# Performance work log

Hardware: AMD Instinct MI355X
Metric: run time of the kernel (lower is better)

Reference implementation:

```python
import jax, jax.numpy as jnp
import numpy as np

B, T, A, H = 2048, 512, 32, 16


def setup_inputs() -> dict:
    key = jax.random.key(0)
    ks = jax.random.split(key, 10)
    s = 1.0 / np.sqrt(H)
    inputs = jax.random.normal(ks[0], (B, T, A), dtype=jnp.float32)
    masks = (jax.random.uniform(ks[1], (B, T)) > 0.05).astype(jnp.float32)
    h0 = jnp.zeros((1, B, H), dtype=jnp.float32)
    c0 = jnp.zeros((1, B, H), dtype=jnp.float32)
    # torch nn.LSTM params (gate order i,f,g,o) and linear heads
    w_ih = jax.random.uniform(ks[2], (4 * H, A), minval=-s, maxval=s)
    w_hh = jax.random.uniform(ks[3], (4 * H, H), minval=-s, maxval=s)
    b_ih = jax.random.uniform(ks[4], (4 * H,), minval=-s, maxval=s)
    b_hh = jax.random.uniform(ks[5], (4 * H,), minval=-s, maxval=s)
    w_actor = jax.random.uniform(ks[6], (A, H), minval=-s, maxval=s)
    b_actor = jax.random.uniform(ks[7], (A,), minval=-s, maxval=s)
    w_critic = jax.random.uniform(ks[8], (1, H), minval=-s, maxval=s)
    b_critic = jax.random.uniform(ks[9], (1,), minval=-s, maxval=s)
    return {"inputs": inputs, "masks": masks, "h0": h0, "c0": c0,
            "w_ih": w_ih, "w_hh": w_hh, "b_ih": b_ih, "b_hh": b_hh,
            "w_actor": w_actor, "b_actor": b_actor,
            "w_critic": w_critic, "b_critic": b_critic}


def reference(inputs, masks, h0, c0, w_ih, w_hh, b_ih, b_hh,
              w_actor, b_actor, w_critic, b_critic):
    # masked LSTM scan: state is zeroed where mask==0 before each step
    def step(carry, xm):
        h, c = carry                      # [B,H]
        x, m = xm                         # x:[B,A], m:[B]
        h = h * m[:, None]
        c = c * m[:, None]
        gates = x @ w_ih.T + b_ih + h @ w_hh.T + b_hh   # [B,4H]
        i, f, g, o = jnp.split(gates, 4, axis=-1)
        i = jax.nn.sigmoid(i)
        f = jax.nn.sigmoid(f)
        g = jnp.tanh(g)
        o = jax.nn.sigmoid(o)
        c2 = f * c + i * g
        h2 = o * jnp.tanh(c2)
        return (h2, c2), h2

    xs = (jnp.swapaxes(inputs, 0, 1), masks.T)          # time-major
    (hT, cT), feats = jax.lax.scan(step, (h0[0], c0[0]), xs)
    feats = jnp.swapaxes(feats, 0, 1)                   # [B,T,H]
    actor = feats @ w_actor.T + b_actor                 # [B,T,A]
    critic = feats @ w_critic.T + b_critic              # [B,T,1]
    return actor, critic, hT[None], cT[None]
```

## Files before the change

kernel.cpp:

```cpp
#include <hip/hip_runtime.h>
#include <stdint.h>

#define Bn 2048
#define Tn 512
#define An 32
#define Hn 16

typedef __attribute__((ext_vector_type(8))) short bf16x8;
typedef __attribute__((ext_vector_type(4))) float f32x4;

union FragU { bf16x8 v; uint32_t u[4]; };

static __device__ __forceinline__ uint32_t pack_hi16(float a, float b){
  return (__float_as_uint(b) & 0xFFFF0000u) | (__float_as_uint(a) >> 16);
}
static __device__ __forceinline__ void split8(const float* s, FragU& hi, FragU& lo){
#pragma unroll
  for (int d = 0; d < 4; ++d){
    float a = s[2*d], b = s[2*d+1];
    float ah = __uint_as_float(__float_as_uint(a) & 0xFFFF0000u);
    float bh = __uint_as_float(__float_as_uint(b) & 0xFFFF0000u);
    hi.u[d] = pack_hi16(a, b);
    lo.u[d] = pack_hi16(a - ah, b - bh);
  }
}
static __device__ __forceinline__ f32x4 MF(const FragU& a, const FragU& b, f32x4 c){
  return __builtin_amdgcn_mfma_f32_16x16x32_bf16(a.v, b.v, c, 0, 0, 0);
}
static __device__ __forceinline__ void packH(const float* hs, uint32_t* pk){
#pragma unroll
  for (int r = 0; r < 4; ++r){
    float hh_ = __uint_as_float(__float_as_uint(hs[r]) & 0xFFFF0000u);
    pk[r] = (__float_as_uint(hs[r] - hh_) & 0xFFFF0000u) | (__float_as_uint(hs[r]) >> 16);
  }
}
static __device__ __forceinline__ void buildB1(const uint32_t* pk, int srcA, int srcB,
                                               uint32_t bsel, FragU& B1){
  uint32_t d0 = (uint32_t)__builtin_amdgcn_ds_bpermute(srcA, (int)pk[0]);
  uint32_t d1 = (uint32_t)__builtin_amdgcn_ds_bpermute(srcA, (int)pk[1]);
  uint32_t d2 = (uint32_t)__builtin_amdgcn_ds_bpermute(srcA, (int)pk[2]);
  uint32_t d3 = (uint32_t)__builtin_amdgcn_ds_bpermute(srcA, (int)pk[3]);
  uint32_t d4 = (uint32_t)__builtin_amdgcn_ds_bpermute(srcB, (int)pk[0]);
  uint32_t d5 = (uint32_t)__builtin_amdgcn_ds_bpermute(srcB, (int)pk[1]);
  uint32_t d6 = (uint32_t)__builtin_amdgcn_ds_bpermute(srcB, (int)pk[2]);
  uint32_t d7 = (uint32_t)__builtin_amdgcn_ds_bpermute(srcB, (int)pk[3]);
  B1.u[0] = __builtin_amdgcn_perm(d1, d0, bsel);
  B1.u[1] = __builtin_amdgcn_perm(d3, d2, bsel);
  B1.u[2] = __builtin_amdgcn_perm(d5, d4, bsel);
  B1.u[3] = __builtin_amdgcn_perm(d7, d6, bsel);
}

__global__ __launch_bounds__(64, 1)
void lstm_fused(const float* __restrict__ xin,
                const float* __restrict__ masks,
                const float* __restrict__ h0,
                const float* __restrict__ c0,
                const float* __restrict__ w_ih,
                const float* __restrict__ w_hh,
                const float* __restrict__ b_ih,
                const float* __restrict__ b_hh,
                const float* __restrict__ w_act,
                const float* __restrict__ b_act,
                const float* __restrict__ w_cr,
                const float* __restrict__ b_cr,
                float* __restrict__ actor,
                float* __restrict__ critic,
                float* __restrict__ hT,
                float* __restrict__ cT)
{
  const int l = threadIdx.x;
  const int q = l >> 4;
  const int n = l & 15;
  const int b0 = blockIdx.x * 16;
  const int colbase = (q & 1) * 8;
  const bool hiQuad = (q < 2);
  const uint32_t bsel = hiQuad ? 0x05040100u : 0x07060302u;

  const float KS = -1.44269504088896f;
  const float KG =  2.88539008177793f;

  FragU wihH0, wihL0, whh10, whh20; f32x4 bias0;
  FragU wihH1, wihL1, whh11, whh21; f32x4 bias1;
  FragU wihH2, wihL2, whh12, whh22; f32x4 bias2;
  FragU wihH3, wihL3, whh13, whh23; f32x4 bias3;
  {
    auto loadGate = [&](int g, float sc, FragU& wh, FragU& wl, FragU& a1, FragU& a2, f32x4& bg){
      float tmp[8];
#pragma unroll
      for (int j = 0; j < 8; ++j) tmp[j] = w_ih[(g*16 + n)*32 + q*8 + j] * sc;
      split8(tmp, wh, wl);
#pragma unroll
      for (int j = 0; j < 8; ++j) tmp[j] = w_hh[(g*16 + n)*16 + colbase + j] * sc;
      FragU hh, hl; split8(tmp, hh, hl);
#pragma unroll
      for (int d = 0; d < 4; ++d){
        a1.u[d] = hh.u[d];
        a2.u[d] = hiQuad ? hl.u[d] : 0u;
      }
#pragma unroll
      for (int r = 0; r < 4; ++r)
        bg[r] = (b_ih[g*16 + q*4 + r] + b_hh[g*16 + q*4 + r]) * sc;
    };
    loadGate(0, KS, wihH0, wihL0, whh10, whh20, bias0);
    loadGate(1, KS, wihH1, wihL1, whh11, whh21, bias1);
    loadGate(2, KG, wihH2, wihL2, whh12, whh22, bias2);
    loadGate(3, KS, wihH3, wihL3, whh13, whh23, bias3);
  }

  FragU whA10, whA20, whA11, whA21, wcA1, wcA2;
  f32x4 biasA0, biasA1;
  const float bcr = b_cr[0];
  {
    float tmp[8];
#pragma unroll
    for (int j = 0; j < 8; ++j) tmp[j] = w_act[(0*16 + n)*16 + colbase + j];
    { FragU hh, hl; split8(tmp, hh, hl);
#pragma unroll
      for (int d = 0; d < 4; ++d){ whA10.u[d] = hh.u[d]; whA20.u[d] = hiQuad ? hl.u[d] : 0u; } }
#pragma unroll
    for (int r = 0; r < 4; ++r) biasA0[r] = b_act[0*16 + q*4 + r];
#pragma unroll
    for (int j = 0; j < 8; ++j) tmp[j] = w_act[(1*16 + n)*16 + colbase + j];
    { FragU hh, hl; split8(tmp, hh, hl);
#pragma unroll
      for (int d = 0; d < 4; ++d){ whA11.u[d] = hh.u[d]; whA21.u[d] = hiQuad ? hl.u[d] : 0u; } }
#pragma unroll
    for (int r = 0; r < 4; ++r) biasA1[r] = b_act[1*16 + q*4 + r];
#pragma unroll
    for (int j = 0; j < 8; ++j) tmp[j] = (n == 0) ? w_cr[colbase + j] : 0.0f;
    { FragU hh, hl; split8(tmp, hh, hl);
#pragma unroll
      for (int d = 0; d < 4; ++d){ wcA1.u[d] = hh.u[d]; wcA2.u[d] = hiQuad ? hl.u[d] : 0u; } }
  }

  const int srcA = (((q & 1) * 2) * 16 + n) * 4;
  const int srcB = srcA + 64;

  float cs[4], hs[4];
#pragma unroll
  for (int r = 0; r < 4; ++r){
    hs[r] = h0[(b0 + n)*16 + q*4 + r];
    cs[r] = c0[(b0 + n)*16 + q*4 + r];
  }
  uint32_t pk[4];
  packH(hs, pk);
  FragU B1;
  buildB1(pk, srcA, srcB, bsel, B1);

  const f32x4 zero4 = {0.f, 0.f, 0.f, 0.f};

  const size_t xrow = (size_t)(b0 + n) * Tn * 32 + q * 8;
  float4 xA[4], xB[4];
#pragma unroll
  for (int u = 0; u < 4; ++u){
    xA[u] = *(const float4*)&xin[xrow + (size_t)u * 32];
    xB[u] = *(const float4*)&xin[xrow + (size_t)u * 32 + 4];
  }
  const size_t mrow = (size_t)(b0 + n) * Tn;
  float4 mQ = *(const float4*)&masks[mrow];

  for (int t0 = 0; t0 < Tn; t0 += 4){
    const int tb = (t0 + 4 < Tn) ? (t0 + 4) : 0;
    float4 mN = *(const float4*)&masks[mrow + tb];
#pragma unroll
    for (int u = 0; u < 4; ++u){
      const int t = t0 + u;
      const float m = (u == 0) ? mQ.x : (u == 1) ? mQ.y : (u == 2) ? mQ.z : mQ.w;
      float cm[4];
#pragma unroll
      for (int r = 0; r < 4; ++r) cm[r] = cs[r] * m;

      FragU Xh, Xl;
      {
        float s[8] = {xA[u].x, xA[u].y, xA[u].z, xA[u].w,
                      xB[u].x, xB[u].y, xB[u].z, xB[u].w};
        split8(s, Xh, Xl);
      }
      {
        const int tn = (t + 4 < Tn) ? (t + 4) : t;
        xA[u] = *(const float4*)&xin[xrow + (size_t)tn * 32];
        xB[u] = *(const float4*)&xin[xrow + (size_t)tn * 32 + 4];
      }

      f32x4 ax0 = MF(wihH0, Xh, bias0); ax0 = MF(wihH0, Xl, ax0); ax0 = MF(wihL0, Xh, ax0);
      f32x4 ax1 = MF(wihH1, Xh, bias1); ax1 = MF(wihH1, Xl, ax1); ax1 = MF(wihL1, Xh, ax1);
      f32x4 ax2 = MF(wihH2, Xh, bias2); ax2 = MF(wihH2, Xl, ax2); ax2 = MF(wihL2, Xh, ax2);
      f32x4 ax3 = MF(wihH3, Xh, bias3); ax3 = MF(wihH3, Xl, ax3); ax3 = MF(wihL3, Xh, ax3);

      f32x4 ah0 = MF(whh10, B1, zero4); ah0 = MF(whh20, B1, ah0);
      f32x4 ah1 = MF(whh11, B1, zero4); ah1 = MF(whh21, B1, ah1);
      f32x4 ah2 = MF(whh12, B1, zero4); ah2 = MF(whh22, B1, ah2);
      f32x4 ah3 = MF(whh13, B1, zero4); ah3 = MF(whh23, B1, ah3);

      if (t){
        const int th = t - 1;
        f32x4 a0 = MF(whA10, B1, biasA0); a0 = MF(whA20, B1, a0);
        *(f32x4*)&actor[((size_t)(b0 + n) * Tn + th) * 32 + 0*16 + q*4] = a0;
        f32x4 a1 = MF(whA11, B1, biasA1); a1 = MF(whA21, B1, a1);
        *(f32x4*)&actor[((size_t)(b0 + n) * Tn + th) * 32 + 1*16 + q*4] = a1;
        f32x4 cc = MF(wcA1, B1, zero4); cc = MF(wcA2, B1, cc);
        if (q == 0) critic[(size_t)(b0 + n) * Tn + th] = cc[0] + bcr;
      }

      float gt[16];
#pragma unroll
      for (int r = 0; r < 4; ++r){
        gt[r]      = ax0[r] + m * ah0[r];
        gt[4 + r]  = ax1[r] + m * ah1[r];
        gt[8 + r]  = ax2[r] + m * ah2[r];
        gt[12 + r] = ax3[r] + m * ah3[r];
      }
      float ex[16];
#pragma unroll
      for (int j = 0; j < 16; ++j) ex[j] = __builtin_amdgcn_exp2f(gt[j]);
#pragma unroll
      for (int j = 0; j < 16; ++j) ex[j] = __builtin_amdgcn_rcpf(1.0f + ex[j]);
      float c2v[4];
#pragma unroll
      for (int r = 0; r < 4; ++r){
        float gv = 1.0f - 2.0f * ex[8 + r];
        c2v[r] = ex[4 + r] * cm[r] + ex[r] * gv;
        cs[r] = c2v[r];
      }
      float et[4];
#pragma unroll
      for (int r = 0; r < 4; ++r) et[r] = __builtin_amdgcn_exp2f(c2v[r] * KG);
#pragma unroll
      for (int r = 0; r < 4; ++r) et[r] = __builtin_amdgcn_rcpf(1.0f + et[r]);
#pragma unroll
      for (int r = 0; r < 4; ++r){
        float ov = ex[12 + r];
        hs[r] = ov - 2.0f * (ov * et[r]);
      }
      packH(hs, pk);
      buildB1(pk, srcA, srcB, bsel, B1);
    }
    mQ = mN;
  }

  {
    const int th = Tn - 1;
    f32x4 a0 = MF(whA10, B1, biasA0); a0 = MF(whA20, B1, a0);
    *(f32x4*)&actor[((size_t)(b0 + n) * Tn + th) * 32 + 0*16 + q*4] = a0;
    f32x4 a1 = MF(whA11, B1, biasA1); a1 = MF(whA21, B1, a1);
    *(f32x4*)&actor[((size_t)(b0 + n) * Tn + th) * 32 + 1*16 + q*4] = a1;
    f32x4 cc = MF(wcA1, B1, zero4); cc = MF(wcA2, B1, cc);
    if (q == 0) critic[(size_t)(b0 + n) * Tn + th] = cc[0] + bcr;
  }
  *(float4*)&hT[(b0 + n)*16 + q*4] = make_float4(hs[0], hs[1], hs[2], hs[3]);
  *(float4*)&cT[(b0 + n)*16 + q*4] = make_float4(cs[0], cs[1], cs[2], cs[3]);
}

extern "C" void kernel_launch(void* const* d_in, const int* in_sizes, int n_in,
                              void* d_out, int out_size, void* d_ws, size_t ws_size,
                              hipStream_t stream) {
  (void)in_sizes; (void)n_in; (void)out_size; (void)d_ws; (void)ws_size;
  const float* xin   = (const float*)d_in[0];
  const float* masks = (const float*)d_in[1];
  const float* h0    = (const float*)d_in[2];
  const float* c0    = (const float*)d_in[3];
  const float* w_ih  = (const float*)d_in[4];
  const float* w_hh  = (const float*)d_in[5];
  const float* b_ih  = (const float*)d_in[6];
  const float* b_hh  = (const float*)d_in[7];
  const float* w_act = (const float*)d_in[8];
  const float* b_act = (const float*)d_in[9];
  const float* w_cr  = (const float*)d_in[10];
  const float* b_cr  = (const float*)d_in[11];

  float* out    = (float*)d_out;
  float* actor  = out;
  float* critic = out + (size_t)Bn * Tn * An;
  float* hT     = critic + (size_t)Bn * Tn;
  float* cT     = hT + (size_t)Bn * Hn;

  lstm_fused<<<Bn/16, 64, 0, stream>>>(xin, masks, h0, c0, w_ih, w_hh, b_ih, b_hh,
                                       w_act, b_act, w_cr, b_cr,
                                       actor, critic, hT, cT);
}
```

Baseline: 535.5 us.

## Use permlane swaps for h broadcast and software-pipeline input projection

Replaces the ds_bpermute-based construction of the recurrent h fragment with v_permlane32/16_swap lane exchanges, guarded by a runtime self-test that falls back to the old path. It also moves the input-projection MFMAs for step t+1 into step t so they overlap the recurrent critical path. The two recurrent MFMA chains are split into independent halves, and the c-state is kept prescaled to shorten the serial dependency chain. The costs are a duplicated loop body (two lambda instantiations, larger code) and higher register pressure from carrying the next step's projections.

```diff
diff --git a/kernel.cpp b/kernel.cpp
--- a/kernel.cpp
+++ b/kernel.cpp
@@ -8,6 +8,7 @@
 
 typedef __attribute__((ext_vector_type(8))) short bf16x8;
 typedef __attribute__((ext_vector_type(4))) float f32x4;
+typedef __attribute__((ext_vector_type(2))) unsigned int uintx2;
 
 union FragU { bf16x8 v; uint32_t u[4]; };
 
@@ -27,15 +28,52 @@
 static __device__ __forceinline__ f32x4 MF(const FragU& a, const FragU& b, f32x4 c){
   return __builtin_amdgcn_mfma_f32_16x16x32_bf16(a.v, b.v, c, 0, 0, 0);
 }
-static __device__ __forceinline__ void packH(const float* hs, uint32_t* pk){
+static __device__ __forceinline__ uint32_t packPair(float h){
+  float hh = __uint_as_float(__float_as_uint(h) & 0xFFFF0000u);
+  float lo = h - hh;
+  return __builtin_amdgcn_perm(__float_as_uint(lo), __float_as_uint(h), 0x07060302u);
+}
+
+static __device__ __forceinline__ void pl32(uint32_t v, uint32_t& x, uint32_t& y){
+#if __has_builtin(__builtin_amdgcn_permlane32_swap)
+  uintx2 s = __builtin_amdgcn_permlane32_swap(v, v, false, false);
+  x = s[0]; y = s[1];
+#else
+  uint32_t a = v, b = v;
+  asm volatile("v_permlane32_swap_b32 %0, %1" : "+v"(a), "+&v"(b));
+  x = a; y = b;
+#endif
+}
+static __device__ __forceinline__ void pl16(uint32_t v, uint32_t& x, uint32_t& y){
+#if __has_builtin(__builtin_amdgcn_permlane16_swap)
+  uintx2 s = __builtin_amdgcn_permlane16_swap(v, v, false, false);
+  x = s[0]; y = s[1];
+#else
+  uint32_t a = v, b = v;
+  asm volatile("v_permlane16_swap_b32 %0, %1" : "+v"(a), "+&v"(b));
+  x = a; y = b;
+#endif
+}
+
+static __device__ __forceinline__ void buildB1perm(const uint32_t* pk, bool qodd,
+                                                   uint32_t bsel, FragU& B1){
+  uint32_t P[4], Q[4];
 #pragma unroll
   for (int r = 0; r < 4; ++r){
-    float hh_ = __uint_as_float(__float_as_uint(hs[r]) & 0xFFFF0000u);
-    pk[r] = (__float_as_uint(hs[r] - hh_) & 0xFFFF0000u) | (__float_as_uint(hs[r]) >> 16);
-  }
-}
-static __device__ __forceinline__ void buildB1(const uint32_t* pk, int srcA, int srcB,
-                                               uint32_t bsel, FragU& B1){
+    uint32_t lo32, hi32; pl32(pk[r], lo32, hi32);
+    uint32_t g0, g1;     pl16(lo32, g0, g1);
+    uint32_t g2, g3;     pl16(hi32, g2, g3);
+    P[r] = qodd ? g2 : g0;
+    Q[r] = qodd ? g3 : g1;
+  }
+  B1.u[0] = __builtin_amdgcn_perm(P[1], P[0], bsel);
+  B1.u[1] = __builtin_amdgcn_perm(P[3], P[2], bsel);
+  B1.u[2] = __builtin_amdgcn_perm(Q[1], Q[0], bsel);
+  B1.u[3] = __builtin_amdgcn_perm(Q[3], Q[2], bsel);
+}
+
+static __device__ __forceinline__ void buildB1ds(const uint32_t* pk, int srcA, int srcB,
+                                                 uint32_t bsel, FragU& B1){
   uint32_t d0 = (uint32_t)__builtin_amdgcn_ds_bpermute(srcA, (int)pk[0]);
   uint32_t d1 = (uint32_t)__builtin_amdgcn_ds_bpermute(srcA, (int)pk[1]);
   uint32_t d2 = (uint32_t)__builtin_amdgcn_ds_bpermute(srcA, (int)pk[2]);
@@ -74,10 +112,22 @@
   const int b0 = blockIdx.x * 16;
   const int colbase = (q & 1) * 8;
   const bool hiQuad = (q < 2);
+  const bool qodd = (q & 1) != 0;
   const uint32_t bsel = hiQuad ? 0x05040100u : 0x07060302u;
 
   const float KS = -1.44269504088896f;
   const float KG =  2.88539008177793f;
+  const float invKG = 0.346573590279973f;
+
+  bool permOK;
+  {
+    uint32_t v = (uint32_t)l;
+    uint32_t x32, y32; pl32(v, x32, y32);
+    uint32_t x16, y16; pl16(v, x16, y16);
+    bool ok = (x32 == (uint32_t)(l & 31)) && (y32 == (uint32_t)(32 | (l & 31))) &&
+              (x16 == (uint32_t)(l & ~16)) && (y16 == (uint32_t)(l | 16));
+    permOK = __all(ok);
+  }
 
   FragU wihH0, wihL0, whh10, whh20; f32x4 bias0;
   FragU wihH1, wihL1, whh11, whh21; f32x4 bias1;
@@ -143,9 +193,9 @@
     cs[r] = c0[(b0 + n)*16 + q*4 + r];
   }
   uint32_t pk[4];
-  packH(hs, pk);
+#pragma unroll
+  for (int r = 0; r < 4; ++r) pk[r] = packPair(hs[r]);
   FragU B1;
-  buildB1(pk, srcA, srcB, bsel, B1);
 
   const f32x4 zero4 = {0.f, 0.f, 0.f, 0.f};
 
@@ -157,85 +207,93 @@
     xB[u] = *(const float4*)&xin[xrow + (size_t)u * 32 + 4];
   }
   const size_t mrow = (size_t)(b0 + n) * Tn;
-  float4 mQ = *(const float4*)&masks[mrow];
-
-  for (int t0 = 0; t0 < Tn; t0 += 4){
-    const int tb = (t0 + 4 < Tn) ? (t0 + 4) : 0;
-    float4 mN = *(const float4*)&masks[mrow + tb];
-#pragma unroll
-    for (int u = 0; u < 4; ++u){
-      const int t = t0 + u;
-      const float m = (u == 0) ? mQ.x : (u == 1) ? mQ.y : (u == 2) ? mQ.z : mQ.w;
-      float cm[4];
-#pragma unroll
-      for (int r = 0; r < 4; ++r) cm[r] = cs[r] * m;
-
-      FragU Xh, Xl;
-      {
-        float s[8] = {xA[u].x, xA[u].y, xA[u].z, xA[u].w,
-                      xB[u].x, xB[u].y, xB[u].z, xB[u].w};
-        split8(s, Xh, Xl);
+  float4 mQ0 = *(const float4*)&masks[mrow];
+
+  auto computeAx = [&](const float4& va, const float4& vb, f32x4* ax){
+    float s[8] = {va.x, va.y, va.z, va.w, vb.x, vb.y, vb.z, vb.w};
+    FragU Xh, Xl; split8(s, Xh, Xl);
+    ax[0] = MF(wihH0, Xh, bias0); ax[0] = MF(wihH0, Xl, ax[0]); ax[0] = MF(wihL0, Xh, ax[0]);
+    ax[1] = MF(wihH1, Xh, bias1); ax[1] = MF(wihH1, Xl, ax[1]); ax[1] = MF(wihL1, Xh, ax[1]);
+    ax[2] = MF(wihH2, Xh, bias2); ax[2] = MF(wihH2, Xl, ax[2]); ax[2] = MF(wihL2, Xh, ax[2]);
+    ax[3] = MF(wihH3, Xh, bias3); ax[3] = MF(wihH3, Xl, ax[3]); ax[3] = MF(wihL3, Xh, ax[3]);
+  };
+
+  auto mainLoop = [&](auto rebuild){
+    rebuild(pk, B1);
+    f32x4 axP[4];
+    computeAx(xA[0], xB[0], axP);
+    float4 mQ = mQ0;
+
+    for (int t0 = 0; t0 < Tn; t0 += 4){
+      const int tb = (t0 + 4 < Tn) ? (t0 + 4) : 0;
+      float4 mN = *(const float4*)&masks[mrow + tb];
+#pragma unroll
+      for (int u = 0; u < 4; ++u){
+        const int t = t0 + u;
+        const float m = (u == 0) ? mQ.x : (u == 1) ? mQ.y : (u == 2) ? mQ.z : mQ.w;
+        float cmk[4];
+#pragma unroll
+        for (int r = 0; r < 4; ++r) cmk[r] = (cs[r] * m) * KG;
+
+        f32x4 ah0a = MF(whh10, B1, zero4), ah0b = MF(whh20, B1, zero4);
+        f32x4 ah1a = MF(whh11, B1, zero4), ah1b = MF(whh21, B1, zero4);
+        f32x4 ah2a = MF(whh12, B1, zero4), ah2b = MF(whh22, B1, zero4);
+        f32x4 ah3a = MF(whh13, B1, zero4), ah3b = MF(whh23, B1, zero4);
+
+        f32x4 a0, a1, cc;
+        if (t){
+          a0 = MF(whA10, B1, biasA0); a0 = MF(whA20, B1, a0);
+          a1 = MF(whA11, B1, biasA1); a1 = MF(whA21, B1, a1);
+          cc = MF(wcA1, B1, zero4);   cc = MF(wcA2, B1, cc);
+        }
+
+        f32x4 axN[4];
+        {
+          const int s2 = (u + 1) & 3;
+          computeAx(xA[s2], xB[s2], axN);
+        }
+        {
+          const int tn = (t + 4 < Tn) ? (t + 4) : t;
+          xA[u] = *(const float4*)&xin[xrow + (size_t)tn * 32];
+          xB[u] = *(const float4*)&xin[xrow + (size_t)tn * 32 + 4];
+        }
+        if (t){
+          const int th = t - 1;
+          *(f32x4*)&actor[((size_t)(b0 + n) * Tn + th) * 32 + 0*16 + q*4] = a0;
+          *(f32x4*)&actor[((size_t)(b0 + n) * Tn + th) * 32 + 1*16 + q*4] = a1;
+          if (q == 0) critic[(size_t)(b0 + n) * Tn + th] = cc[0] + bcr;
+        }
+
+#pragma unroll
+        for (int r = 0; r < 4; ++r){
+          float gi = m * ah0b[r] + axP[0][r]; gi = m * ah0a[r] + gi;
+          float gf = m * ah1b[r] + axP[1][r]; gf = m * ah1a[r] + gf;
+          float gg = m * ah2b[r] + axP[2][r]; gg = m * ah2a[r] + gg;
+          float go = m * ah3b[r] + axP[3][r]; go = m * ah3a[r] + go;
+          float iv = __builtin_amdgcn_rcpf(1.0f + __builtin_amdgcn_exp2f(gi));
+          float fv = __builtin_amdgcn_rcpf(1.0f + __builtin_amdgcn_exp2f(gf));
+          float gr = __builtin_amdgcn_rcpf(1.0f + __builtin_amdgcn_exp2f(gg));
+          float ov = __builtin_amdgcn_rcpf(1.0f + __builtin_amdgcn_exp2f(go));
+          float gvk = gr * (-2.0f * KG) + KG;
+          float c2k = iv * gvk + fv * cmk[r];
+          cs[r] = c2k * invKG;
+          float et = __builtin_amdgcn_rcpf(1.0f + __builtin_amdgcn_exp2f(c2k));
+          float hv = ov - 2.0f * (ov * et);
+          hs[r] = hv;
+          pk[r] = packPair(hv);
+        }
+        rebuild(pk, B1);
+#pragma unroll
+        for (int g = 0; g < 4; ++g) axP[g] = axN[g];
       }
-      {
-        const int tn = (t + 4 < Tn) ? (t + 4) : t;
-        xA[u] = *(const float4*)&xin[xrow + (size_t)tn * 32];
-        xB[u] = *(const float4*)&xin[xrow + (size_t)tn * 32 + 4];
-      }
-
-      f32x4 ax0 = MF(wihH0, Xh, bias0); ax0 = MF(wihH0, Xl, ax0); ax0 = MF(wihL0, Xh, ax0);
-      f32x4 ax1 = MF(wihH1, Xh, bias1); ax1 = MF(wihH1, Xl, ax1); ax1 = MF(wihL1, Xh, ax1);
-      f32x4 ax2 = MF(wihH2, Xh, bias2); ax2 = MF(wihH2, Xl, ax2); ax2 = MF(wihL2, Xh, ax2);
-      f32x4 ax3 = MF(wihH3, Xh, bias3); ax3 = MF(wihH3, Xl, ax3); ax3 = MF(wihL3, Xh, ax3);
-
-      f32x4 ah0 = MF(whh10, B1, zero4); ah0 = MF(whh20, B1, ah0);
-      f32x4 ah1 = MF(whh11, B1, zero4); ah1 = MF(whh21, B1, ah1);
-      f32x4 ah2 = MF(whh12, B1, zero4); ah2 = MF(whh22, B1, ah2);
-      f32x4 ah3 = MF(whh13, B1, zero4); ah3 = MF(whh23, B1, ah3);
-
-      if (t){
-        const int th = t - 1;
-        f32x4 a0 = MF(whA10, B1, biasA0); a0 = MF(whA20, B1, a0);
-        *(f32x4*)&actor[((size_t)(b0 + n) * Tn + th) * 32 + 0*16 + q*4] = a0;
-        f32x4 a1 = MF(whA11, B1, biasA1); a1 = MF(whA21, B1, a1);
-        *(f32x4*)&actor[((size_t)(b0 + n) * Tn + th) * 32 + 1*16 + q*4] = a1;
-        f32x4 cc = MF(wcA1, B1, zero4); cc = MF(wcA2, B1, cc);
-        if (q == 0) critic[(size_t)(b0 + n) * Tn + th] = cc[0] + bcr;
-      }
-
-      float gt[16];
-#pragma unroll
-      for (int r = 0; r < 4; ++r){
-        gt[r]      = ax0[r] + m * ah0[r];
-        gt[4 + r]  = ax1[r] + m * ah1[r];
-        gt[8 + r]  = ax2[r] + m * ah2[r];
-        gt[12 + r] = ax3[r] + m * ah3[r];
-      }
-      float ex[16];
-#pragma unroll
-      for (int j = 0; j < 16; ++j) ex[j] = __builtin_amdgcn_exp2f(gt[j]);
-#pragma unroll
-      for (int j = 0; j < 16; ++j) ex[j] = __builtin_amdgcn_rcpf(1.0f + ex[j]);
-      float c2v[4];
-#pragma unroll
-      for (int r = 0; r < 4; ++r){
-        float gv = 1.0f - 2.0f * ex[8 + r];
-        c2v[r] = ex[4 + r] * cm[r] + ex[r] * gv;
-        cs[r] = c2v[r];
-      }
-      float et[4];
-#pragma unroll
-      for (int r = 0; r < 4; ++r) et[r] = __builtin_amdgcn_exp2f(c2v[r] * KG);
-#pragma unroll
-      for (int r = 0; r < 4; ++r) et[r] = __builtin_amdgcn_rcpf(1.0f + et[r]);
-#pragma unroll
-      for (int r = 0; r < 4; ++r){
-        float ov = ex[12 + r];
-        hs[r] = ov - 2.0f * (ov * et[r]);
-      }
-      packH(hs, pk);
-      buildB1(pk, srcA, srcB, bsel, B1);
+      mQ = mN;
     }
-    mQ = mN;
+  };
+
+  if (permOK){
+    mainLoop([&](const uint32_t* p, FragU& B){ buildB1perm(p, qodd, bsel, B); });
+  } else {
+    mainLoop([&](const uint32_t* p, FragU& B){ buildB1ds(p, srcA, srcB, bsel, B); });
   }
 
   {
```

Result: slower. 636.6 us (+18.9%).
